# Optimization experiments

Measured on AMD Instinct MI355X. Metric: run time of the kernel, lower is better.

Reference implementation:

```python
import jax, jax.numpy as jnp
import numpy as np

N, C_IN, C_OUT, P, W, H = 32, 32, 16, 4, 16, 16
D = P * P
EPS = 1e-6


def squash(s, axis=-1):
    # v = ||s||^2/(1+||s||^2) * s/||s||, eps-stabilized as in the repo (eps=1e-6)
    n2 = jnp.sum(s * s, axis=axis, keepdims=True)
    n = jnp.sqrt(n2)
    return (n2 / (1.0 + n2)) * s / (n + EPS)


def setup_inputs() -> dict:
    key = jax.random.key(0)
    k1, k2, k3 = jax.random.split(key, 3)
    l = jax.random.normal(k1, (N, C_IN, D, W, H), jnp.float32)
    g = jax.random.normal(k2, (N, C_OUT, D), jnp.float32)
    weight = jax.random.normal(k3, (1, C_IN, 1, C_OUT, P, P), jnp.float32)
    return {"l": l, "g": g, "weight": weight, "num_iters": 3}


def reference(l, g, weight, num_iters):
    n, c, d, w, h = l.shape
    p = weight.shape[-1]
    c_out = weight.shape[3]
    # (N, C, D, W, H) -> (N, C, W*H, P, P)
    lp = jnp.transpose(l, (0, 1, 3, 4, 2)).reshape(n, c, w * h, p, p)
    # votes: pose matmul against per-(in,out) transform matrices
    # v[n,c,s,o] = lp[n,c,s] @ weight[0,c,0,o]   -> (N, C, WH, C_out, P, P)
    v = jnp.einsum('ncsij,cojk->ncsoik', lp, weight[0, :, 0])
    M = c * w * h
    v = v.reshape(n, M, c_out, d)          # (N, M, C_out, D)
    g = g[:, None, :, :]                    # (N, 1, C_out, D)
    # dynamic routing, logits initialized from agreement with the prior global capsule g
    b = jnp.sum(v * g, axis=-1, keepdims=True)   # (N, M, C_out, 1)
    cc = None
    for _ in range(num_iters):
        cc = jax.nn.softmax(b, axis=1)           # attention over input votes M
        g = squash(jnp.sum(cc * v, axis=1, keepdims=True))  # (N, 1, C_out, D)
        b = b + jnp.sum(v * g, axis=-1, keepdims=True)
    a = jnp.squeeze(cc, -1)   # (N, M, C_out)
    g = jnp.squeeze(g, 1)     # (N, C_out, D)
    return a, g
```

## Files before the change

### kernel.cpp

```cpp
#include <hip/hip_runtime.h>
#include <math.h>

#define N_   32
#define CIN  32
#define COUT 16
#define D_   16
#define S_   256
#define M_   (CIN * S_)
#define NBLK (N_ * CIN)

#define LOG2E 1.4426950408889634f

#define PROW 20
#define PIDX(n, c, o) ((((size_t)(n) * CIN + (c)) * COUT + (o)) * PROW)

#define BSLOT 64

__device__ __forceinline__ float2 aload_f2(const float* p) {
  unsigned long long v = __hip_atomic_load(
      (const unsigned long long*)p, __ATOMIC_RELAXED, __HIP_MEMORY_SCOPE_AGENT);
  float2 r;
  r.x = __uint_as_float((unsigned)v);
  r.y = __uint_as_float((unsigned)(v >> 32));
  return r;
}
__device__ __forceinline__ void astore_f2(float* p, float a, float b) {
  unsigned long long v =
      ((unsigned long long)__float_as_uint(b) << 32) | __float_as_uint(a);
  __hip_atomic_store((unsigned long long*)p, v, __ATOMIC_RELAXED,
                     __HIP_MEMORY_SCOPE_AGENT);
}

#define SW(s) ((((s) & 3)) ^ (((s) >> 2) & 3))

__device__ __forceinline__ void stage_tile(const float* __restrict__ gsrc,
                                           float* ls, int tid) {
  const float4* src = (const float4*)gsrc;
#pragma unroll
  for (int j = 0; j < 4; j++) {
    int f = ((tid & 3) << 6) + (tid >> 2) + (j << 8);
    float4 val = src[f];
    int dd = f >> 6;
    int u  = f & 63;
    int chunk = dd >> 2, lo = dd & 3;
    float vv[4] = {val.x, val.y, val.z, val.w};
#pragma unroll
    for (int m = 0; m < 4; m++) {
      int s = (u << 2) + m;
      int p = chunk ^ SW(s);
      ls[(s << 4) + (p << 2) + lo] = vv[m];
    }
  }
}

__device__ __forceinline__ void read_lp(const float* ls, int s, float* lp) {
  const float4* row = (const float4*)(ls + (s << 4));
  int sw = SW(s);
#pragma unroll
  for (int c = 0; c < 4; c++) {
    float4 q = row[c ^ sw];
    lp[c * 4 + 0] = q.x; lp[c * 4 + 1] = q.y;
    lp[c * 4 + 2] = q.z; lp[c * 4 + 3] = q.w;
  }
}

__device__ __forceinline__ float dot16(const float* a, const float* b) {
  float a0 = 0.f, a1 = 0.f, a2 = 0.f, a3 = 0.f;
#pragma unroll
  for (int k = 0; k < 4; k++) {
    a0 = fmaf(a[k],      b[k],      a0);
    a1 = fmaf(a[4 + k],  b[4 + k],  a1);
    a2 = fmaf(a[8 + k],  b[8 + k],  a2);
    a3 = fmaf(a[12 + k], b[12 + k], a3);
  }
  return (a0 + a1) + (a2 + a3);
}

__device__ __forceinline__ void gbarrier(int* bar, int idx, int n, int tid) {
  __syncthreads();
  if (tid == 0) {
    int* base = bar + ((idx << 5) + n) * BSLOT;
    if (__hip_atomic_fetch_add(base, 1, __ATOMIC_RELAXED,
                               __HIP_MEMORY_SCOPE_AGENT) == CIN - 1) {
      __hip_atomic_store(base + 32, 1, __ATOMIC_RELAXED,
                         __HIP_MEMORY_SCOPE_AGENT);
    } else {
      int guard = 0;
      while (__hip_atomic_load(base + 32, __ATOMIC_RELAXED,
                               __HIP_MEMORY_SCOPE_AGENT) == 0) {
        __builtin_amdgcn_s_sleep(2);
        if (++guard > 5000000) break;
      }
    }
  }
  __syncthreads();
}

template <int PASS>
__device__ __forceinline__ void routing_pass(
    int n, int c, int tid, int o, int strip,
    const float* __restrict__ wgt,
    const float* __restrict__ part_in, float* __restrict__ part_out,
    const float* ls, float red[4][18][16], float red2[18][16],
    float hd[16][20], float* Gacc, float& shift) {
  if constexpr (PASS > 0) {
    if (tid < 64) {
      const int ho = tid & 15, hs = tid >> 4;
      float H[18];
#pragma unroll
      for (int f = 0; f < 17; f++) H[f] = 0.f;
      H[17] = -INFINITY;
#pragma unroll 4
      for (int q = 0; q < 8; q++) {
        const float* r = part_in + PIDX(n, hs + 4 * q, ho);
#pragma unroll
        for (int i = 0; i < 8; i++) {
          float2 v = aload_f2(r + 2 * i);
          H[2 * i + 0] += v.x;
          H[2 * i + 1] += v.y;
        }
        float2 t = aload_f2(r + 16);
        H[16] += t.x;
        H[17] = fmaxf(H[17], t.y);
      }
#pragma unroll
      for (int off = 16; off <= 32; off <<= 1) {
#pragma unroll
        for (int f = 0; f < 17; f++) H[f] += __shfl_xor(H[f], off);
        H[17] = fmaxf(H[17], __shfl_xor(H[17], off));
      }
      if (tid < 16) {
        float inv = 1.0f / H[16], n2 = 0.f, Sg[16];
#pragma unroll
        for (int d = 0; d < 16; d++) { Sg[d] = H[d] * inv; n2 = fmaf(Sg[d], Sg[d], n2); }
        float coef = n2 / ((1.f + n2) * (sqrtf(n2) + 1e-6f));
        float4* hq = (float4*)hd[tid];
#pragma unroll
        for (int i = 0; i < 4; i++)
          hq[i] = make_float4(coef * Sg[i * 4 + 0], coef * Sg[i * 4 + 1],
                              coef * Sg[i * 4 + 2], coef * Sg[i * 4 + 3]);
        hd[tid][16] = H[17];
      }
    }
    __syncthreads();
    const float4* hq = (const float4*)hd[o];
#pragma unroll
    for (int i = 0; i < 4; i++) {
      float4 v = hq[i];
      Gacc[i * 4 + 0] += v.x; Gacc[i * 4 + 1] += v.y;
      Gacc[i * 4 + 2] += v.z; Gacc[i * 4 + 3] += v.w;
    }
    shift = hd[o][16];
  }

  float WG[16];
  {
    float wreg[16];
    const float4* wp = (const float4*)(wgt + (c * COUT + o) * 16);
#pragma unroll
    for (int i = 0; i < 4; i++) {
      float4 t = wp[i];
      wreg[i * 4 + 0] = t.x; wreg[i * 4 + 1] = t.y;
      wreg[i * 4 + 2] = t.z; wreg[i * 4 + 3] = t.w;
    }
#pragma unroll
    for (int i = 0; i < 4; i++)
#pragma unroll
      for (int j = 0; j < 4; j++) {
        float acc = 0.f;
#pragma unroll
        for (int k = 0; k < 4; k++)
          acc = fmaf(wreg[j * 4 + k], Gacc[i * 4 + k], acc);
        WG[i * 4 + j] = acc * LOG2E;
      }
  }

  float se = 0.f, bmx = -INFINITY, E[16];
#pragma unroll
  for (int d = 0; d < 16; d++) E[d] = 0.f;

#pragma unroll 4
  for (int it = 0; it < 16; it++) {
    float lp[16];
    read_lp(ls, strip + (it << 4), lp);
    float b = dot16(lp, WG) - shift;
    float e = exp2f(b);
    bmx = fmaxf(bmx, b);
    se += e;
#pragma unroll
    for (int d = 0; d < 16; d++) E[d] = fmaf(e, lp[d], E[d]);
  }

#pragma unroll
  for (int off = 16; off <= 32; off <<= 1) {
    se += __shfl_xor(se, off);
    bmx = fmaxf(bmx, __shfl_xor(bmx, off));
#pragma unroll
    for (int d = 0; d < 16; d++) E[d] += __shfl_xor(E[d], off);
  }

  const int w = tid >> 6;
  if ((tid & 63) < 16) {
#pragma unroll
    for (int d = 0; d < 16; d++) red[w][d][o] = E[d];
    red[w][16][o] = se;
    red[w][17][o] = bmx;
  }
  __syncthreads();

  for (int p = tid; p < 288; p += 256) {
    int f = p >> 4, oo = p & 15;
    float v0 = red[0][f][oo], v1 = red[1][f][oo];
    float v2 = red[2][f][oo], v3 = red[3][f][oo];
    red2[f][oo] = (f == 17) ? fmaxf(fmaxf(v0, v1), fmaxf(v2, v3))
                            : ((v0 + v1) + (v2 + v3));
  }
  __syncthreads();

  if (tid < 16) {
    float wt[16];
    const float4* wp = (const float4*)(wgt + (c * COUT + tid) * 16);
#pragma unroll
    for (int i = 0; i < 4; i++) {
      float4 t = wp[i];
      wt[i * 4 + 0] = t.x; wt[i * 4 + 1] = t.y;
      wt[i * 4 + 2] = t.z; wt[i * 4 + 3] = t.w;
    }
    float Et[16];
#pragma unroll
    for (int d = 0; d < 16; d++) Et[d] = red2[d][tid];
    float* p0 = part_out + PIDX(n, c, tid);
#pragma unroll
    for (int i = 0; i < 4; i++) {
      float s0 = 0.f, s1 = 0.f, s2 = 0.f, s3 = 0.f;
#pragma unroll
      for (int j = 0; j < 4; j++) {
        s0 = fmaf(Et[i * 4 + j], wt[j * 4 + 0], s0);
        s1 = fmaf(Et[i * 4 + j], wt[j * 4 + 1], s1);
        s2 = fmaf(Et[i * 4 + j], wt[j * 4 + 2], s2);
        s3 = fmaf(Et[i * 4 + j], wt[j * 4 + 3], s3);
      }
      astore_f2(p0 + 4 * i + 0, s0, s1);
      astore_f2(p0 + 4 * i + 2, s2, s3);
    }
    astore_f2(p0 + 16, red2[16][tid], red2[17][tid] + shift);
  }
}

__global__ __launch_bounds__(256)
__attribute__((amdgpu_waves_per_eu(4, 4))) void fused_kernel(
    const float* __restrict__ l, const float* __restrict__ wgt,
    const float* __restrict__ g0, float* __restrict__ a_out,
    float* __restrict__ g_out, float* __restrict__ PB0,
    float* __restrict__ PB1, int* __restrict__ bar) {
  const int bid = blockIdx.x;
  const int n = bid >> 5;
  const int c = bid & 31;
  const int tid = threadIdx.x;
  const int o = tid & 15;
  const int strip = tid >> 4;

  __shared__ float ls[D_ * S_];
  __shared__ float red[4][18][16];
  __shared__ float red2[18][16];
  __shared__ float hd[16][20];
  __shared__ float sinv[16];

  stage_tile(l + ((size_t)(n * CIN + c)) * D_ * S_, ls, tid);

  float Gacc[16];
  {
    const float4* gp = (const float4*)(g0 + (n * COUT + o) * 16);
#pragma unroll
    for (int i = 0; i < 4; i++) {
      float4 u = gp[i];
      Gacc[i * 4 + 0] = u.x; Gacc[i * 4 + 1] = u.y;
      Gacc[i * 4 + 2] = u.z; Gacc[i * 4 + 3] = u.w;
    }
  }

  __syncthreads();

  float shift = 0.f;

  routing_pass<0>(n, c, tid, o, strip, wgt, nullptr, PB0, ls, red, red2, hd,
                  Gacc, shift);
  gbarrier(bar, 0, n, tid);
  routing_pass<1>(n, c, tid, o, strip, wgt, PB0, PB1, ls, red, red2, hd,
                  Gacc, shift);
  gbarrier(bar, 1, n, tid);
  routing_pass<2>(n, c, tid, o, strip, wgt, PB1, PB0, ls, red, red2, hd,
                  Gacc, shift);
  gbarrier(bar, 2, n, tid);

  if (tid < 64) {
    const int ho = tid & 15, hs = tid >> 4;
    float H[17];
#pragma unroll
    for (int f = 0; f < 17; f++) H[f] = 0.f;
#pragma unroll 4
    for (int q = 0; q < 8; q++) {
      const float* r = PB0 + PIDX(n, hs + 4 * q, ho);
#pragma unroll
      for (int i = 0; i < 8; i++) {
        float2 v = aload_f2(r + 2 * i);
        H[2 * i + 0] += v.x;
        H[2 * i + 1] += v.y;
      }
      H[16] += aload_f2(r + 16).x;
    }
#pragma unroll
    for (int off = 16; off <= 32; off <<= 1) {
#pragma unroll
      for (int f = 0; f < 17; f++) H[f] += __shfl_xor(H[f], off);
    }
    if (tid < 16) {
      float inv = 1.0f / H[16];
      sinv[tid] = inv;
      if (c == 0) {
        float n2 = 0.f, Sg[16];
#pragma unroll
        for (int d = 0; d < 16; d++) { Sg[d] = H[d] * inv; n2 = fmaf(Sg[d], Sg[d], n2); }
        float coef = n2 / ((1.f + n2) * (sqrtf(n2) + 1e-6f));
        float* go = g_out + (n * COUT + tid) * 16;
#pragma unroll
        for (int d = 0; d < 16; d++) go[d] = coef * Sg[d];
      }
    }
  }
  __syncthreads();

  float WG[16];
  {
    float wreg[16];
    const float4* wp = (const float4*)(wgt + (c * COUT + o) * 16);
#pragma unroll
    for (int i = 0; i < 4; i++) {
      float4 t = wp[i];
      wreg[i * 4 + 0] = t.x; wreg[i * 4 + 1] = t.y;
      wreg[i * 4 + 2] = t.z; wreg[i * 4 + 3] = t.w;
    }
#pragma unroll
    for (int i = 0; i < 4; i++)
#pragma unroll
      for (int j = 0; j < 4; j++) {
        float acc = 0.f;
#pragma unroll
        for (int k = 0; k < 4; k++)
          acc = fmaf(wreg[j * 4 + k], Gacc[i * 4 + k], acc);
        WG[i * 4 + j] = acc * LOG2E;
      }
  }
  const float myinv = sinv[o];
  float* abase = a_out + ((size_t)(n * M_ + c * S_)) * COUT;
#pragma unroll 4
  for (int it = 0; it < 16; it++) {
    float lp[16];
    read_lp(ls, strip + (it << 4), lp);
    float b = dot16(lp, WG) - shift;
    abase[(size_t)((strip + (it << 4)) * COUT + o)] = exp2f(b) * myinv;
  }
}

extern "C" void kernel_launch(void* const* d_in, const int* in_sizes, int n_in,
                              void* d_out, int out_size, void* d_ws, size_t ws_size,
                              hipStream_t stream) {
  const float* l = (const float*)d_in[0];
  const float* g = (const float*)d_in[1];
  const float* w = (const float*)d_in[2];

  float* out = (float*)d_out;
  float* a_out = out;
  float* g_out = out + (size_t)N_ * M_ * COUT;

  float* ws = (float*)d_ws;
  float* PB0 = ws;
  float* PB1 = ws + (size_t)N_ * CIN * COUT * PROW;
  int* bar = (int*)(ws + 2 * (size_t)N_ * CIN * COUT * PROW);

  hipMemsetAsync(bar, 0, 3 * N_ * BSLOT * sizeof(int), stream);

  fused_kernel<<<NBLK, 256, 0, stream>>>(l, w, g, a_out, g_out, PB0, PB1, bar);
}
```

Baseline: 136.3 us.

## Have last-arriving block reduce partials and publish routing state per batch

Reworks the per-batch barrier so the last-arriving block reduces all 32 partial rows, computes the squashed capsule and a log-sum shift, and publishes them to a small buffer. Waiting blocks then read 17 floats instead of each redundantly reducing all partials. This removes the max tracking in favour of a log2(sum) shift and uses a single partial buffer. It also trims the reduction arrays and changes the launch bounds. The cost is a serialized reduction on the leader, during which the other blocks sit idle.

```diff
diff --git a/kernel.cpp b/kernel.cpp
--- a/kernel.cpp
+++ b/kernel.cpp
@@ -14,7 +14,13 @@
 #define PROW 20
 #define PIDX(n, c, o) ((((size_t)(n) * CIN + (c)) * COUT + (o)) * PROW)
 
+#define PUBROW 20
+#define PUBIDX(n, o) ((((size_t)(n) * COUT) + (o)) * PUBROW)
+
 #define BSLOT 64
+
+#define WS_PB  6144
+#define WS_PUB (6144 + 327680)
 
 __device__ __forceinline__ float2 aload_f2(const float* p) {
   unsigned long long v = __hip_atomic_load(
@@ -76,15 +82,188 @@
   return (a0 + a1) + (a2 + a3);
 }
 
-__device__ __forceinline__ void gbarrier(int* bar, int idx, int n, int tid) {
+__device__ __forceinline__ void build_WG(const float* __restrict__ wgt, int c,
+                                         int o, const float* Gacc, float* WG) {
+  float wreg[16];
+  const float4* wp = (const float4*)(wgt + (c * COUT + o) * 16);
+#pragma unroll
+  for (int i = 0; i < 4; i++) {
+    float4 t = wp[i];
+    wreg[i * 4 + 0] = t.x; wreg[i * 4 + 1] = t.y;
+    wreg[i * 4 + 2] = t.z; wreg[i * 4 + 3] = t.w;
+  }
+#pragma unroll
+  for (int i = 0; i < 4; i++)
+#pragma unroll
+    for (int j = 0; j < 4; j++) {
+      float acc = 0.f;
+#pragma unroll
+      for (int k = 0; k < 4; k++)
+        acc = fmaf(wreg[j * 4 + k], Gacc[i * 4 + k], acc);
+      WG[i * 4 + j] = acc * LOG2E;
+    }
+}
+
+__device__ __forceinline__ void sweep_store(
+    int n, int c, int tid, int o, int strip,
+    const float* __restrict__ wgt, float* __restrict__ PB,
+    const float* ls, float red[4][17][16], float red2[17][16],
+    const float* Gacc, float shift) {
+  float WG[16];
+  build_WG(wgt, c, o, Gacc, WG);
+
+  float se = 0.f, E[16];
+#pragma unroll
+  for (int d = 0; d < 16; d++) E[d] = 0.f;
+
+#pragma unroll 4
+  for (int it = 0; it < 16; it++) {
+    float lp[16];
+    read_lp(ls, strip + (it << 4), lp);
+    float e = exp2f(dot16(lp, WG) - shift);
+    se += e;
+#pragma unroll
+    for (int d = 0; d < 16; d++) E[d] = fmaf(e, lp[d], E[d]);
+  }
+
+#pragma unroll
+  for (int off = 16; off <= 32; off <<= 1) {
+    se += __shfl_xor(se, off);
+#pragma unroll
+    for (int d = 0; d < 16; d++) E[d] += __shfl_xor(E[d], off);
+  }
+
+  const int w = tid >> 6;
+  if ((tid & 63) < 16) {
+#pragma unroll
+    for (int d = 0; d < 16; d++) red[w][d][o] = E[d];
+    red[w][16][o] = se;
+  }
+  __syncthreads();
+
+  for (int p = tid; p < 272; p += 256) {
+    int f = p >> 4, oo = p & 15;
+    red2[f][oo] = ((red[0][f][oo] + red[1][f][oo]) +
+                   (red[2][f][oo] + red[3][f][oo]));
+  }
+  __syncthreads();
+
+  if (tid < 16) {
+    float wt[16];
+    const float4* wp = (const float4*)(wgt + (c * COUT + tid) * 16);
+#pragma unroll
+    for (int i = 0; i < 4; i++) {
+      float4 t = wp[i];
+      wt[i * 4 + 0] = t.x; wt[i * 4 + 1] = t.y;
+      wt[i * 4 + 2] = t.z; wt[i * 4 + 3] = t.w;
+    }
+    float Et[16];
+#pragma unroll
+    for (int d = 0; d < 16; d++) Et[d] = red2[d][tid];
+    float* p0 = PB + PIDX(n, c, tid);
+#pragma unroll
+    for (int i = 0; i < 4; i++) {
+      float s0 = 0.f, s1 = 0.f, s2 = 0.f, s3 = 0.f;
+#pragma unroll
+      for (int j = 0; j < 4; j++) {
+        s0 = fmaf(Et[i * 4 + j], wt[j * 4 + 0], s0);
+        s1 = fmaf(Et[i * 4 + j], wt[j * 4 + 1], s1);
+        s2 = fmaf(Et[i * 4 + j], wt[j * 4 + 2], s2);
+        s3 = fmaf(Et[i * 4 + j], wt[j * 4 + 3], s3);
+      }
+      astore_f2(p0 + 4 * i + 0, s0, s1);
+      astore_f2(p0 + 4 * i + 2, s2, s3);
+    }
+    astore_f2(p0 + 16, red2[16][tid], 0.f);
+  }
+}
+
+template <int SLOT, bool FINAL>
+__device__ __forceinline__ void exchange(
+    int n, int tid, const float* __restrict__ PB, float* __restrict__ pub,
+    float* __restrict__ g_out, int* __restrict__ bar,
+    float red[4][17][16], float hd[16][20], float* sinv, int* lead) {
   __syncthreads();
   if (tid == 0) {
-    int* base = bar + ((idx << 5) + n) * BSLOT;
-    if (__hip_atomic_fetch_add(base, 1, __ATOMIC_RELAXED,
-                               __HIP_MEMORY_SCOPE_AGENT) == CIN - 1) {
+    int* base = bar + ((SLOT << 5) + n) * BSLOT;
+    *lead = (__hip_atomic_fetch_add(base, 1, __ATOMIC_RELAXED,
+                                    __HIP_MEMORY_SCOPE_AGENT) == CIN - 1);
+  }
+  __syncthreads();
+
+  if (*lead) {
+    const int l = tid & 63, w = tid >> 6;
+    const int ho = l & 15, hs = l >> 4;
+    float H[17];
+#pragma unroll
+    for (int f = 0; f < 17; f++) H[f] = 0.f;
+#pragma unroll
+    for (int j = 0; j < 2; j++) {
+      const float* r = PB + PIDX(n, hs + 4 * (2 * w + j), ho);
+#pragma unroll
+      for (int i = 0; i < 8; i++) {
+        float2 v = aload_f2(r + 2 * i);
+        H[2 * i + 0] += v.x;
+        H[2 * i + 1] += v.y;
+      }
+      H[16] += aload_f2(r + 16).x;
+    }
+#pragma unroll
+    for (int off = 16; off <= 32; off <<= 1)
+#pragma unroll
+      for (int f = 0; f < 17; f++) H[f] += __shfl_xor(H[f], off);
+    if (l < 16) {
+#pragma unroll
+      for (int f = 0; f < 17; f++) red[w][f][ho] = H[f];
+    }
+    __syncthreads();
+    if (tid < 16) {
+      float S[16], se;
+#pragma unroll
+      for (int f = 0; f < 16; f++)
+        S[f] = (red[0][f][tid] + red[1][f][tid]) +
+               (red[2][f][tid] + red[3][f][tid]);
+      se = (red[0][16][tid] + red[1][16][tid]) +
+           (red[2][16][tid] + red[3][16][tid]);
+      float inv = 1.0f / se;
+      if (FINAL) {
+        sinv[tid] = inv;
+        __hip_atomic_store(pub + PUBIDX(n, tid), inv, __ATOMIC_RELAXED,
+                           __HIP_MEMORY_SCOPE_AGENT);
+        float n2 = 0.f, Sg[16];
+#pragma unroll
+        for (int d = 0; d < 16; d++) { Sg[d] = S[d] * inv; n2 = fmaf(Sg[d], Sg[d], n2); }
+        float coef = n2 / ((1.f + n2) * (sqrtf(n2) + 1e-6f));
+        float* go = g_out + (n * COUT + tid) * 16;
+#pragma unroll
+        for (int d = 0; d < 16; d++) go[d] = coef * Sg[d];
+      } else {
+        float n2 = 0.f, Sg[16];
+#pragma unroll
+        for (int d = 0; d < 16; d++) { Sg[d] = S[d] * inv; n2 = fmaf(Sg[d], Sg[d], n2); }
+        float coef = n2 / ((1.f + n2) * (sqrtf(n2) + 1e-6f));
+        float Dsh = __log2f(se);
+        float* hrow = hd[tid];
+        float* prow = pub + PUBIDX(n, tid);
+#pragma unroll
+        for (int i = 0; i < 8; i++) {
+          float a = coef * Sg[2 * i], b = coef * Sg[2 * i + 1];
+          hrow[2 * i] = a; hrow[2 * i + 1] = b;
+          astore_f2(prow + 2 * i, a, b);
+        }
+        hrow[16] = Dsh;
+        astore_f2(prow + 16, Dsh, 0.f);
+      }
+    }
+    __syncthreads();
+    if (tid == 0) {
+      int* base = bar + ((SLOT << 5) + n) * BSLOT;
       __hip_atomic_store(base + 32, 1, __ATOMIC_RELAXED,
                          __HIP_MEMORY_SCOPE_AGENT);
-    } else {
+    }
+  } else {
+    if (tid == 0) {
+      int* base = bar + ((SLOT << 5) + n) * BSLOT;
       int guard = 0;
       while (__hip_atomic_load(base + 32, __ATOMIC_RELAXED,
                                __HIP_MEMORY_SCOPE_AGENT) == 0) {
@@ -92,167 +271,32 @@
         if (++guard > 5000000) break;
       }
     }
-  }
-  __syncthreads();
-}
-
-template <int PASS>
-__device__ __forceinline__ void routing_pass(
-    int n, int c, int tid, int o, int strip,
-    const float* __restrict__ wgt,
-    const float* __restrict__ part_in, float* __restrict__ part_out,
-    const float* ls, float red[4][18][16], float red2[18][16],
-    float hd[16][20], float* Gacc, float& shift) {
-  if constexpr (PASS > 0) {
-    if (tid < 64) {
-      const int ho = tid & 15, hs = tid >> 4;
-      float H[18];
-#pragma unroll
-      for (int f = 0; f < 17; f++) H[f] = 0.f;
-      H[17] = -INFINITY;
-#pragma unroll 4
-      for (int q = 0; q < 8; q++) {
-        const float* r = part_in + PIDX(n, hs + 4 * q, ho);
+    __syncthreads();
+    if (FINAL) {
+      if (tid < 16)
+        sinv[tid] = __hip_atomic_load(pub + PUBIDX(n, tid), __ATOMIC_RELAXED,
+                                      __HIP_MEMORY_SCOPE_AGENT);
+    } else {
+      if (tid < 16) {
+        const float* prow = pub + PUBIDX(n, tid);
+        float* hrow = hd[tid];
 #pragma unroll
         for (int i = 0; i < 8; i++) {
-          float2 v = aload_f2(r + 2 * i);
-          H[2 * i + 0] += v.x;
-          H[2 * i + 1] += v.y;
+          float2 v = aload_f2(prow + 2 * i);
+          hrow[2 * i] = v.x; hrow[2 * i + 1] = v.y;
         }
-        float2 t = aload_f2(r + 16);
-        H[16] += t.x;
-        H[17] = fmaxf(H[17], t.y);
-      }
-#pragma unroll
-      for (int off = 16; off <= 32; off <<= 1) {
-#pragma unroll
-        for (int f = 0; f < 17; f++) H[f] += __shfl_xor(H[f], off);
-        H[17] = fmaxf(H[17], __shfl_xor(H[17], off));
-      }
-      if (tid < 16) {
-        float inv = 1.0f / H[16], n2 = 0.f, Sg[16];
-#pragma unroll
-        for (int d = 0; d < 16; d++) { Sg[d] = H[d] * inv; n2 = fmaf(Sg[d], Sg[d], n2); }
-        float coef = n2 / ((1.f + n2) * (sqrtf(n2) + 1e-6f));
-        float4* hq = (float4*)hd[tid];
-#pragma unroll
-        for (int i = 0; i < 4; i++)
-          hq[i] = make_float4(coef * Sg[i * 4 + 0], coef * Sg[i * 4 + 1],
-                              coef * Sg[i * 4 + 2], coef * Sg[i * 4 + 3]);
-        hd[tid][16] = H[17];
+        hrow[16] = aload_f2(prow + 16).x;
       }
     }
     __syncthreads();
-    const float4* hq = (const float4*)hd[o];
-#pragma unroll
-    for (int i = 0; i < 4; i++) {
-      float4 v = hq[i];
-      Gacc[i * 4 + 0] += v.x; Gacc[i * 4 + 1] += v.y;
-      Gacc[i * 4 + 2] += v.z; Gacc[i * 4 + 3] += v.w;
-    }
-    shift = hd[o][16];
-  }
-
-  float WG[16];
-  {
-    float wreg[16];
-    const float4* wp = (const float4*)(wgt + (c * COUT + o) * 16);
-#pragma unroll
-    for (int i = 0; i < 4; i++) {
-      float4 t = wp[i];
-      wreg[i * 4 + 0] = t.x; wreg[i * 4 + 1] = t.y;
-      wreg[i * 4 + 2] = t.z; wreg[i * 4 + 3] = t.w;
-    }
-#pragma unroll
-    for (int i = 0; i < 4; i++)
-#pragma unroll
-      for (int j = 0; j < 4; j++) {
-        float acc = 0.f;
-#pragma unroll
-        for (int k = 0; k < 4; k++)
-          acc = fmaf(wreg[j * 4 + k], Gacc[i * 4 + k], acc);
-        WG[i * 4 + j] = acc * LOG2E;
-      }
-  }
-
-  float se = 0.f, bmx = -INFINITY, E[16];
-#pragma unroll
-  for (int d = 0; d < 16; d++) E[d] = 0.f;
-
-#pragma unroll 4
-  for (int it = 0; it < 16; it++) {
-    float lp[16];
-    read_lp(ls, strip + (it << 4), lp);
-    float b = dot16(lp, WG) - shift;
-    float e = exp2f(b);
-    bmx = fmaxf(bmx, b);
-    se += e;
-#pragma unroll
-    for (int d = 0; d < 16; d++) E[d] = fmaf(e, lp[d], E[d]);
-  }
-
-#pragma unroll
-  for (int off = 16; off <= 32; off <<= 1) {
-    se += __shfl_xor(se, off);
-    bmx = fmaxf(bmx, __shfl_xor(bmx, off));
-#pragma unroll
-    for (int d = 0; d < 16; d++) E[d] += __shfl_xor(E[d], off);
-  }
-
-  const int w = tid >> 6;
-  if ((tid & 63) < 16) {
-#pragma unroll
-    for (int d = 0; d < 16; d++) red[w][d][o] = E[d];
-    red[w][16][o] = se;
-    red[w][17][o] = bmx;
-  }
-  __syncthreads();
-
-  for (int p = tid; p < 288; p += 256) {
-    int f = p >> 4, oo = p & 15;
-    float v0 = red[0][f][oo], v1 = red[1][f][oo];
-    float v2 = red[2][f][oo], v3 = red[3][f][oo];
-    red2[f][oo] = (f == 17) ? fmaxf(fmaxf(v0, v1), fmaxf(v2, v3))
-                            : ((v0 + v1) + (v2 + v3));
-  }
-  __syncthreads();
-
-  if (tid < 16) {
-    float wt[16];
-    const float4* wp = (const float4*)(wgt + (c * COUT + tid) * 16);
-#pragma unroll
-    for (int i = 0; i < 4; i++) {
-      float4 t = wp[i];
-      wt[i * 4 + 0] = t.x; wt[i * 4 + 1] = t.y;
-      wt[i * 4 + 2] = t.z; wt[i * 4 + 3] = t.w;
-    }
-    float Et[16];
-#pragma unroll
-    for (int d = 0; d < 16; d++) Et[d] = red2[d][tid];
-    float* p0 = part_out + PIDX(n, c, tid);
-#pragma unroll
-    for (int i = 0; i < 4; i++) {
-      float s0 = 0.f, s1 = 0.f, s2 = 0.f, s3 = 0.f;
-#pragma unroll
-      for (int j = 0; j < 4; j++) {
-        s0 = fmaf(Et[i * 4 + j], wt[j * 4 + 0], s0);
-        s1 = fmaf(Et[i * 4 + j], wt[j * 4 + 1], s1);
-        s2 = fmaf(Et[i * 4 + j], wt[j * 4 + 2], s2);
-        s3 = fmaf(Et[i * 4 + j], wt[j * 4 + 3], s3);
-      }
-      astore_f2(p0 + 4 * i + 0, s0, s1);
-      astore_f2(p0 + 4 * i + 2, s2, s3);
-    }
-    astore_f2(p0 + 16, red2[16][tid], red2[17][tid] + shift);
-  }
-}
-
-__global__ __launch_bounds__(256)
-__attribute__((amdgpu_waves_per_eu(4, 4))) void fused_kernel(
+  }
+}
+
+__global__ __launch_bounds__(256, 4) void fused_kernel(
     const float* __restrict__ l, const float* __restrict__ wgt,
     const float* __restrict__ g0, float* __restrict__ a_out,
-    float* __restrict__ g_out, float* __restrict__ PB0,
-    float* __restrict__ PB1, int* __restrict__ bar) {
+    float* __restrict__ g_out, float* __restrict__ PB,
+    float* __restrict__ pub, int* __restrict__ bar) {
   const int bid = blockIdx.x;
   const int n = bid >> 5;
   const int c = bid & 31;
@@ -261,10 +305,11 @@
   const int strip = tid >> 4;
 
   __shared__ float ls[D_ * S_];
-  __shared__ float red[4][18][16];
-  __shared__ float red2[18][16];
+  __shared__ float red[4][17][16];
+  __shared__ float red2[17][16];
   __shared__ float hd[16][20];
   __shared__ float sinv[16];
+  __shared__ int lead;
 
   stage_tile(l + ((size_t)(n * CIN + c)) * D_ * S_, ls, tid);
 
@@ -283,74 +328,37 @@
 
   float shift = 0.f;
 
-  routing_pass<0>(n, c, tid, o, strip, wgt, nullptr, PB0, ls, red, red2, hd,
-                  Gacc, shift);
-  gbarrier(bar, 0, n, tid);
-  routing_pass<1>(n, c, tid, o, strip, wgt, PB0, PB1, ls, red, red2, hd,
-                  Gacc, shift);
-  gbarrier(bar, 1, n, tid);
-  routing_pass<2>(n, c, tid, o, strip, wgt, PB1, PB0, ls, red, red2, hd,
-                  Gacc, shift);
-  gbarrier(bar, 2, n, tid);
-
-  if (tid < 64) {
-    const int ho = tid & 15, hs = tid >> 4;
-    float H[17];
-#pragma unroll
-    for (int f = 0; f < 17; f++) H[f] = 0.f;
-#pragma unroll 4
-    for (int q = 0; q < 8; q++) {
-      const float* r = PB0 + PIDX(n, hs + 4 * q, ho);
-#pragma unroll
-      for (int i = 0; i < 8; i++) {
-        float2 v = aload_f2(r + 2 * i);
-        H[2 * i + 0] += v.x;
-        H[2 * i + 1] += v.y;
-      }
-      H[16] += aload_f2(r + 16).x;
-    }
-#pragma unroll
-    for (int off = 16; off <= 32; off <<= 1) {
-#pragma unroll
-      for (int f = 0; f < 17; f++) H[f] += __shfl_xor(H[f], off);
-    }
-    if (tid < 16) {
-      float inv = 1.0f / H[16];
-      sinv[tid] = inv;
-      if (c == 0) {
-        float n2 = 0.f, Sg[16];
-#pragma unroll
-        for (int d = 0; d < 16; d++) { Sg[d] = H[d] * inv; n2 = fmaf(Sg[d], Sg[d], n2); }
-        float coef = n2 / ((1.f + n2) * (sqrtf(n2) + 1e-6f));
-        float* go = g_out + (n * COUT + tid) * 16;
-#pragma unroll
-        for (int d = 0; d < 16; d++) go[d] = coef * Sg[d];
-      }
-    }
-  }
-  __syncthreads();
+  sweep_store(n, c, tid, o, strip, wgt, PB, ls, red, red2, Gacc, shift);
+  exchange<0, false>(n, tid, PB, pub, g_out, bar, red, hd, sinv, &lead);
+  {
+    const float4* hq = (const float4*)hd[o];
+#pragma unroll
+    for (int i = 0; i < 4; i++) {
+      float4 v = hq[i];
+      Gacc[i * 4 + 0] += v.x; Gacc[i * 4 + 1] += v.y;
+      Gacc[i * 4 + 2] += v.z; Gacc[i * 4 + 3] += v.w;
+    }
+    shift += hd[o][16];
+  }
+
+  sweep_store(n, c, tid, o, strip, wgt, PB, ls, red, red2, Gacc, shift);
+  exchange<1, false>(n, tid, PB, pub, g_out, bar, red, hd, sinv, &lead);
+  {
+    const float4* hq = (const float4*)hd[o];
+#pragma unroll
+    for (int i = 0; i < 4; i++) {
+      float4 v = hq[i];
+      Gacc[i * 4 + 0] += v.x; Gacc[i * 4 + 1] += v.y;
+      Gacc[i * 4 + 2] += v.z; Gacc[i * 4 + 3] += v.w;
+    }
+    shift += hd[o][16];
+  }
+
+  sweep_store(n, c, tid, o, strip, wgt, PB, ls, red, red2, Gacc, shift);
+  exchange<2, true>(n, tid, PB, pub, g_out, bar, red, hd, sinv, &lead);
 
   float WG[16];
-  {
-    float wreg[16];
-    const float4* wp = (const float4*)(wgt + (c * COUT + o) * 16);
-#pragma unroll
-    for (int i = 0; i < 4; i++) {
-      float4 t = wp[i];
-      wreg[i * 4 + 0] = t.x; wreg[i * 4 + 1] = t.y;
-      wreg[i * 4 + 2] = t.z; wreg[i * 4 + 3] = t.w;
-    }
-#pragma unroll
-    for (int i = 0; i < 4; i++)
-#pragma unroll
-      for (int j = 0; j < 4; j++) {
-        float acc = 0.f;
-#pragma unroll
-        for (int k = 0; k < 4; k++)
-          acc = fmaf(wreg[j * 4 + k], Gacc[i * 4 + k], acc);
-        WG[i * 4 + j] = acc * LOG2E;
-      }
-  }
+  build_WG(wgt, c, o, Gacc, WG);
   const float myinv = sinv[o];
   float* abase = a_out + ((size_t)(n * M_ + c * S_)) * COUT;
 #pragma unroll 4
@@ -374,11 +382,11 @@
   float* g_out = out + (size_t)N_ * M_ * COUT;
 
   float* ws = (float*)d_ws;
-  float* PB0 = ws;
-  float* PB1 = ws + (size_t)N_ * CIN * COUT * PROW;
-  int* bar = (int*)(ws + 2 * (size_t)N_ * CIN * COUT * PROW);
+  int* bar = (int*)ws;
+  float* PB = ws + WS_PB;
+  float* pub = ws + WS_PUB;
 
   hipMemsetAsync(bar, 0, 3 * N_ * BSLOT * sizeof(int), stream);
 
-  fused_kernel<<<NBLK, 256, 0, stream>>>(l, w, g, a_out, g_out, PB0, PB1, bar);
-}
+  fused_kernel<<<NBLK, 256, 0, stream>>>(l, w, g, a_out, g_out, PB, pub, bar);
+}
```

Result: faster. 133.6 us (-2.0%).
